# Optimization experiments

Hardware: AMD Instinct MI355X
Metric: run time of the kernel (lower is better)

The kernel has to match this reference:

```python
import jax, jax.numpy as jnp
import numpy as np

N_NODES = 100000
N_GRAPHS = 64


def gcn_conv(x, src, dst, W, b, num_nodes):
    """PyG GCNConv: add self-loops, symmetric deg normalization, aggregate at dst."""
    h = x @ W  # [N, out]
    ones_e = jnp.ones(src.shape[0], dtype=x.dtype)
    # degree includes self-loop (+1)
    deg = jax.ops.segment_sum(ones_e, dst, num_segments=num_nodes) + 1.0
    dinv = jnp.where(deg > 0, 1.0 / jnp.sqrt(deg), 0.0)  # deg>=1 always here
    norm = dinv[src] * dinv[dst]  # [E]
    msg = h[src] * norm[:, None]  # gather + scale
    agg = jax.ops.segment_sum(msg, dst, num_segments=num_nodes)
    # self-loop contribution: norm_ii = dinv[i]^2
    agg = agg + h * (dinv * dinv)[:, None]
    return agg + b


def global_mean_pool(x, batch, num_graphs):
    sums = jax.ops.segment_sum(x, batch, num_segments=num_graphs)
    counts = jax.ops.segment_sum(jnp.ones(x.shape[0], dtype=x.dtype), batch,
                                 num_segments=num_graphs)
    return sums / jnp.maximum(counts, 1.0)[:, None]


def setup_inputs() -> dict:
    key = jax.random.key(0)
    ks = jax.random.split(key, 8)
    H = 128
    x = jax.random.normal(ks[0], (N_NODES, 4), dtype=jnp.float32)
    edge_index = jax.random.randint(ks[1], (2, 1600000), 0, N_NODES, dtype=jnp.int64 if jax.config.read('jax_enable_x64') else jnp.int32)
    batch = jnp.sort(jax.random.randint(ks[2], (N_NODES,), 0, N_GRAPHS))
    def glorot(k, shape):
        fan_in, fan_out = shape
        lim = np.sqrt(6.0 / (fan_in + fan_out))
        return jax.random.uniform(k, shape, jnp.float32, -lim, lim)
    return {
        'x': x,
        'edge_index': edge_index,
        'batch': batch,
        'W1': glorot(ks[3], (4, H)), 'b1': jnp.zeros((H,), jnp.float32),
        'W2': glorot(ks[4], (H, H)), 'b2': jnp.zeros((H,), jnp.float32),
        'W3': glorot(ks[5], (H, H)), 'b3': jnp.zeros((H,), jnp.float32),
        'Wl': glorot(ks[6], (H, 2)), 'bl': jnp.zeros((2,), jnp.float32),
    }


def reference(x, edge_index, batch, W1, b1, W2, b2, W3, b3, Wl, bl):
    src, dst = edge_index[0], edge_index[1]
    h = jax.nn.relu(gcn_conv(x, src, dst, W1, b1, N_NODES))
    h = jax.nn.relu(gcn_conv(h, src, dst, W2, b2, N_NODES))
    h = jax.nn.relu(gcn_conv(h, src, dst, W3, b3, N_NODES))
    g = global_mean_pool(h, batch, N_GRAPHS)  # [G, H]
    logits = g @ Wl + bl  # [G, 2]
    return jax.nn.log_softmax(logits, axis=1)
```

## Files before the change

kernel.cpp:

```cpp
#include <hip/hip_runtime.h>

#define HDIM 128
#define NGRAPH 64

#define BSHIFT 9
#define NBUCK 196
#define BCAP 84
#define BSTR 85
#define RCAP 9216
#define BIN_CHUNK 8192

typedef __attribute__((ext_vector_type(8))) short short8;
typedef __attribute__((ext_vector_type(4))) float floatx4;
typedef __attribute__((ext_vector_type(2))) float floatx2;
typedef __attribute__((ext_vector_type(4))) unsigned int uintx4;

__device__ __forceinline__ float bf2f(unsigned short u) {
    union { unsigned int i; float f; } v;
    v.i = ((unsigned int)u) << 16;
    return v.f;
}
__device__ __forceinline__ unsigned short f2bf(float f) {
    unsigned int u = __float_as_uint(f);
    u += 0x7FFFu + ((u >> 16) & 1u);
    return (unsigned short)(u >> 16);
}


__global__ __launch_bounds__(256) void k_misc(int* __restrict__ gcur,
                                              const int* __restrict__ batch,
                                              float* __restrict__ gcnt,
                                              float* __restrict__ gsum,
                                              const float* __restrict__ W2,
                                              unsigned short* __restrict__ Wp2,
                                              const float* __restrict__ W3,
                                              unsigned short* __restrict__ Wp3,
                                              int N, int nbuck) {
    int t = threadIdx.x;
    int blk = blockIdx.x;
    if (blk == 0) {
        if (t < nbuck) gcur[t] = t * RCAP;
        for (int i = t; i < NGRAPH * 128; i += 256) gsum[i] = 0.f;
        if (t < NGRAPH) {
            int g = t;
            int lo = 0, hi = N;
            while (lo < hi) { int m = (lo + hi) >> 1; if (batch[m] < g) lo = m + 1; else hi = m; }
            int lb = lo;
            lo = 0; hi = N;
            while (lo < hi) { int m = (lo + hi) >> 1; if (batch[m] < g + 1) lo = m + 1; else hi = m; }
            gcnt[g] = (float)(lo - lb);
        }
        return;
    }
    const float* W = (blk <= 64) ? W2 : W3;
    unsigned short* Wp = (blk <= 64) ? Wp2 : Wp3;
    int idx = ((blk <= 64) ? (blk - 1) : (blk - 65)) * 256 + t;
    int j = idx & 7, l = (idx >> 3) & 63, frag = idx >> 9;
    int c = frag >> 2, ks = frag & 3;
    int k = ks * 32 + ((l >> 4) & 3) * 8 + j;
    int n = c * 16 + (l & 15);
    Wp[idx] = f2bf(W[k * 128 + n]);
}


__global__ __launch_bounds__(256) void k_binA(const int* __restrict__ src,
                                              const int* __restrict__ dst,
                                              int* __restrict__ gcur,
                                              unsigned int* __restrict__ binned, int E) {
    __shared__ unsigned int bin[NBUCK * BSTR];
    __shared__ int bcnt[NBUCK];
    __shared__ int bbase[NBUCK];
    int t = threadIdx.x;
    for (int b = t; b < NBUCK; b += 256) bcnt[b] = 0;
    __syncthreads();
    int e0 = blockIdx.x * BIN_CHUNK;
    #pragma unroll
    for (int i = 0; i < BIN_CHUNK / 1024; i++) {
        int e = e0 + i * 1024 + t * 4;
        if (e + 3 < E) {
            const int4 d4 = *(const int4*)&dst[e];
            const int4 s4 = *(const int4*)&src[e];
            int dd[4] = {d4.x, d4.y, d4.z, d4.w};
            int ss[4] = {s4.x, s4.y, s4.z, s4.w};
            #pragma unroll
            for (int k = 0; k < 4; k++) {
                int d = dd[k];
                unsigned int rec = ((unsigned int)(d & 511) << 20) | (unsigned int)ss[k];
                int b = d >> BSHIFT;
                int idx = atomicAdd(&bcnt[b], 1);
                if (idx < BCAP) bin[b * BSTR + idx] = rec;
                else { int p = atomicAdd(&gcur[b], 1); binned[p] = rec; }
            }
        } else {
            for (int k = 0; k < 4; k++) {
                int e2 = e + k;
                if (e2 < E) {
                    int d = dst[e2];
                    unsigned int rec = ((unsigned int)(d & 511) << 20) | (unsigned int)src[e2];
                    int b = d >> BSHIFT;
                    int idx = atomicAdd(&bcnt[b], 1);
                    if (idx < BCAP) bin[b * BSTR + idx] = rec;
                    else { int p = atomicAdd(&gcur[b], 1); binned[p] = rec; }
                }
            }
        }
    }
    __syncthreads();
    if (t < NBUCK) {
        int cnt = min(bcnt[t], BCAP);
        bbase[t] = atomicAdd(&gcur[t], cnt);
    }
    __syncthreads();
    int wave = t >> 6, lane = t & 63;
    for (int b = wave; b < NBUCK; b += 4) {
        int cnt = min(bcnt[b], BCAP);
        int base = bbase[b];
        for (int j = lane; j < cnt; j += 64) binned[base + j] = bin[b * BSTR + j];
    }
}

__global__ __launch_bounds__(256) void k_fillB(const int* __restrict__ gcur,
                                               const unsigned int* __restrict__ binned,
                                               int* __restrict__ P,
                                               float* __restrict__ dinv,
                                               int* __restrict__ csr,
                                               const float4* __restrict__ x4,
                                               float4* __restrict__ xs4,
                                               int N, int nbuck) {
    __shared__ int ps[256];
    __shared__ int cnt[512];
    __shared__ int image[RCAP];
    int b = blockIdx.x;
    int t = threadIdx.x;
    int lt = (t < nbuck) ? (gcur[t] - t * RCAP) : 0;
    ps[t] = lt;
    __syncthreads();
    for (int d = 1; d < 256; d <<= 1) {
        int o = (t >= d) ? ps[t - d] : 0;
        __syncthreads();
        ps[t] += o;
        __syncthreads();
    }
    int start = (b > 0) ? ps[b - 1] : 0;
    int len = ps[b] - start;
    __syncthreads();

    int n0 = b << BSHIFT;
    int nloc = min(n0 + 512, N) - n0;
    cnt[t] = 0; cnt[t + 256] = 0;
    __syncthreads();
    const unsigned int* rb = binned + (size_t)b * RCAP;
    for (int i = t; i < len; i += 256) atomicAdd(&cnt[rb[i] >> 20], 1);
    __syncthreads();
    int c0 = cnt[2 * t], c1 = cnt[2 * t + 1];
    int pair = c0 + c1;
    __syncthreads();
    cnt[t] = pair;
    __syncthreads();
    for (int d = 1; d < 256; d <<= 1) {
        int o = (t >= d) ? cnt[t - d] : 0;
        __syncthreads();
        cnt[t] += o;
        __syncthreads();
    }
    int excl = cnt[t] - pair;
    __syncthreads();
    if (2 * t < nloc) {
        int n = n0 + 2 * t;
        float dv0 = rsqrtf((float)c0 + 1.0f);
        P[n] = start + excl;
        dinv[n] = dv0;
        float4 xv = x4[n];
        xs4[n] = make_float4(xv.x * dv0, xv.y * dv0, xv.z * dv0, xv.w * dv0);
    }
    if (2 * t + 1 < nloc) {
        int n = n0 + 2 * t + 1;
        float dv1 = rsqrtf((float)c1 + 1.0f);
        P[n] = start + excl + c0;
        dinv[n] = dv1;
        float4 xv = x4[n];
        xs4[n] = make_float4(xv.x * dv1, xv.y * dv1, xv.z * dv1, xv.w * dv1);
    }
    if (b == nbuck - 1 && t == 0) P[N] = start + len;
    cnt[2 * t] = excl;
    cnt[2 * t + 1] = excl + c0;
    __syncthreads();
    for (int i = t; i < len; i += 256) {
        unsigned int rec = rb[i];
        int pos = atomicAdd(&cnt[rec >> 20], 1);
        image[pos] = (int)(rec & 0xFFFFFu);
    }
    __syncthreads();
    for (int i = t; i < len; i += 256) csr[start + i] = image[i];
}

#define LXS 136
#define LFPS 144
__global__ __launch_bounds__(256) void k_l1t2(const int* __restrict__ P,
                                              const int* __restrict__ csr,
                                              const float4* __restrict__ xs,
                                              const float* __restrict__ W1,
                                              const float* __restrict__ b1,
                                              const unsigned short* __restrict__ Wp,
                                              const float* __restrict__ dinv,
                                              unsigned char* __restrict__ out8, int N) {
    __shared__ unsigned short lx[64 * LXS];
    __shared__ unsigned short lw[16384];
    __shared__ float w1s[512];
    __shared__ float b1s[128];
    __shared__ float ax[64][4];
    int t = threadIdx.x;
    int n0 = blockIdx.x * 64;

    for (int i = t; i < 512; i += 256) w1s[i] = W1[i];
    if (t < 128) b1s[t] = b1[t];
    for (int ch = t; ch < 2048; ch += 256)
        *(uint4*)&lw[ch * 8] = *(const uint4*)&Wp[ch * 8];

    {
        int d = n0 + (t >> 2), l = t & 3;
        float axx = 0.f, ayy = 0.f, azz = 0.f, aww = 0.f;
        if (d < N) {
            int s0 = P[d], s1 = P[d + 1];
            int i = s0 + l;
            for (; i + 4 < s1; i += 8) {
                int e0 = csr[i], e1 = csr[i + 4];
                float4 v0 = xs[e0], v1 = xs[e1];
                axx += v0.x + v1.x; ayy += v0.y + v1.y;
                azz += v0.z + v1.z; aww += v0.w + v1.w;
            }
            if (i < s1) {
                float4 v = xs[csr[i]];
                axx += v.x; ayy += v.y; azz += v.z; aww += v.w;
            }
        }
        axx += __shfl_xor(axx, 1); ayy += __shfl_xor(ayy, 1);
        azz += __shfl_xor(azz, 1); aww += __shfl_xor(aww, 1);
        axx += __shfl_xor(axx, 2); ayy += __shfl_xor(ayy, 2);
        azz += __shfl_xor(azz, 2); aww += __shfl_xor(aww, 2);
        if (l == 0) {
            int nl = t >> 2;
            if (d < N) {
                float dd = dinv[d];
                float4 sv = xs[d];
                ax[nl][0] = (axx + sv.x * dd) * dd;
                ax[nl][1] = (ayy + sv.y * dd) * dd;
                ax[nl][2] = (azz + sv.z * dd) * dd;
                ax[nl][3] = (aww + sv.w * dd) * dd;
            } else {
                ax[nl][0] = 0.f; ax[nl][1] = 0.f; ax[nl][2] = 0.f; ax[nl][3] = 0.f;
            }
        }
    }
    __syncthreads();

    for (int i = t; i < 8192; i += 256) {
        int n = i >> 7, j = i & 127;
        float v = b1s[j] + ax[n][0] * w1s[j] + ax[n][1] * w1s[128 + j]
                         + ax[n][2] * w1s[256 + j] + ax[n][3] * w1s[384 + j];
        lx[n * LXS + j] = f2bf(fmaxf(v, 0.f));
    }
    __syncthreads();

    int w = t >> 6, lane = t & 63;
    int m0 = w * 16;
    int col = lane & 15, quad = lane >> 4;

    short8 afrag[4];
    #pragma unroll
    for (int ks = 0; ks < 4; ks++)
        afrag[ks] = *(const short8*)&lx[(m0 + col) * LXS + ks * 32 + quad * 8];

    float dv[4];
    #pragma unroll
    for (int r = 0; r < 4; r++) {
        int gn = n0 + m0 + quad * 4 + r;
        dv[r] = (gn < N) ? dinv[gn] : 0.0f;
    }
    __syncthreads();
    unsigned char* lfp = (unsigned char*)lx;

    #pragma unroll
    for (int c = 0; c < 8; c++) {
        floatx4 acc = {0.f, 0.f, 0.f, 0.f};
        #pragma unroll
        for (int ks = 0; ks < 4; ks++) {
            const short8 bfrag = *(const short8*)&lw[((c * 4 + ks) * 64 + lane) * 8];
            acc = __builtin_amdgcn_mfma_f32_16x16x32_bf16(afrag[ks], bfrag, acc, 0, 0, 0);
        }
        int j = c * 16 + col;
        #pragma unroll
        for (int r = 0; r < 4; r++) {
            int nl = m0 + quad * 4 + r;
            float v = acc[r] * dv[r];
            lfp[nl * LFPS + j] =
                (unsigned char)(__builtin_amdgcn_cvt_pk_fp8_f32(v, v, 0, false) & 0xFF);
        }
    }
    __syncthreads();
    #pragma unroll
    for (int k = 0; k < 2; k++) {
        int ch = t + k * 256;
        int s = ch >> 7;
        int idx2 = ch & 127;
        int nl = idx2 >> 1;
        int k0 = (idx2 & 1) * 16;
        int gn = n0 + nl;
        if (gn < N)
            *(uintx4*)&out8[(size_t)s * N * 32 + (size_t)gn * 32 + k0] =
                *(const uintx4*)&lfp[nl * LFPS + s * 32 + k0];
    }
}

__global__ __launch_bounds__(256) void k_transform_mfma(const unsigned short* __restrict__ in,
                                                        const unsigned short* __restrict__ Wp,
                                                        const float* __restrict__ dinv,
                                                        unsigned char* __restrict__ out8, int N) {
    __shared__ unsigned short lx[64 * LXS];
    __shared__ unsigned short lw[16384];
    int t = threadIdx.x;
    int n0 = blockIdx.x * 64;

    for (int ch = t; ch < 1024; ch += 256) {
        int row = ch >> 4, part = ch & 15;
        uint4 val = make_uint4(0, 0, 0, 0);
        if (n0 + row < N) val = *(const uint4*)&in[(size_t)(n0 + row) * 128 + part * 8];
        *(uint4*)&lx[row * LXS + part * 8] = val;
    }
    for (int ch = t; ch < 2048; ch += 256)
        *(uint4*)&lw[ch * 8] = *(const uint4*)&Wp[ch * 8];
    __syncthreads();

    int w = t >> 6, lane = t & 63;
    int m0 = w * 16;
    int col = lane & 15, quad = lane >> 4;

    short8 afrag[4];
    #pragma unroll
    for (int ks = 0; ks < 4; ks++)
        afrag[ks] = *(const short8*)&lx[(m0 + col) * LXS + ks * 32 + quad * 8];

    float dv[4];
    #pragma unroll
    for (int r = 0; r < 4; r++) {
        int gn = n0 + m0 + quad * 4 + r;
        dv[r] = (gn < N) ? dinv[gn] : 0.0f;
    }
    __syncthreads();
    unsigned char* lfp = (unsigned char*)lx;

    #pragma unroll
    for (int c = 0; c < 8; c++) {
        floatx4 acc = {0.f, 0.f, 0.f, 0.f};
        #pragma unroll
        for (int ks = 0; ks < 4; ks++) {
            const short8 bfrag = *(const short8*)&lw[((c * 4 + ks) * 64 + lane) * 8];
            acc = __builtin_amdgcn_mfma_f32_16x16x32_bf16(afrag[ks], bfrag, acc, 0, 0, 0);
        }
        int j = c * 16 + col;
        #pragma unroll
        for (int r = 0; r < 4; r++) {
            int nl = m0 + quad * 4 + r;
            float v = acc[r] * dv[r];
            lfp[nl * LFPS + j] =
                (unsigned char)(__builtin_amdgcn_cvt_pk_fp8_f32(v, v, 0, false) & 0xFF);
        }
    }
    __syncthreads();
    #pragma unroll
    for (int k = 0; k < 2; k++) {
        int ch = t + k * 256;
        int s = ch >> 7;
        int idx2 = ch & 127;
        int nl = idx2 >> 1;
        int k0 = (idx2 & 1) * 16;
        int gn = n0 + nl;
        if (gn < N)
            *(uintx4*)&out8[(size_t)s * N * 32 + (size_t)gn * 32 + k0] =
                *(const uintx4*)&lfp[nl * LFPS + s * 32 + k0];
    }
}

__device__ __forceinline__ void dec8x2(uint4 u, floatx2* a) {
    a[0] += __builtin_amdgcn_cvt_pk_f32_fp8(u.x, false);
    a[1] += __builtin_amdgcn_cvt_pk_f32_fp8(u.x, true);
    a[2] += __builtin_amdgcn_cvt_pk_f32_fp8(u.y, false);
    a[3] += __builtin_amdgcn_cvt_pk_f32_fp8(u.y, true);
    a[4] += __builtin_amdgcn_cvt_pk_f32_fp8(u.z, false);
    a[5] += __builtin_amdgcn_cvt_pk_f32_fp8(u.z, true);
    a[6] += __builtin_amdgcn_cvt_pk_f32_fp8(u.w, false);
    a[7] += __builtin_amdgcn_cvt_pk_f32_fp8(u.w, true);
}

__global__ __launch_bounds__(256) void k_agg_sl(const int* __restrict__ P,
                                                const int* __restrict__ csr,
                                                const unsigned int* __restrict__ tab,
                                                const float* __restrict__ dinv,
                                                const float* __restrict__ bias,
                                                unsigned short* __restrict__ out16,
                                                const int* __restrict__ batch,
                                                float* __restrict__ gsum,
                                                int N, int mode) {
    __shared__ float psum[32][32];
    int t = threadIdx.x;
    int bid = blockIdx.x;
    int xcd = bid & 7;
    int slice = xcd >> 1;
    int chunk = (bid >> 3) * 2 + (xcd & 1);
    int nb = chunk * 32;
    int grp = t >> 3;
    int lg = t & 7;
    int slot = lg >> 1;
    int half = lg & 1;
    int g = nb + grp;
    const unsigned int* sl = tab + (size_t)slice * N * 8;
    int hofs = half * 4;

    floatx2 a2[8];
    #pragma unroll
    for (int j = 0; j < 8; j++) a2[j] = (floatx2){0.f, 0.f};

    if (g < N) {
        int s0 = P[g], s1 = P[g + 1];
        int i = s0;
        for (; i + 8 <= s1; i += 8) {
            int e0 = csr[i + slot];
            int e1 = csr[i + slot + 4];
            uint4 u0 = *(const uint4*)&sl[(size_t)e0 * 8 + hofs];
            uint4 u1 = *(const uint4*)&sl[(size_t)e1 * 8 + hofs];
            dec8x2(u0, a2);
            dec8x2(u1, a2);
        }
        if (i + 4 <= s1) {
            int e = csr[i + slot];
            uint4 u = *(const uint4*)&sl[(size_t)e * 8 + hofs];
            dec8x2(u, a2);
            i += 4;
        }
        int k = i + slot;
        if (k < s1) {
            int e = csr[k];
            uint4 u = *(const uint4*)&sl[(size_t)e * 8 + hofs];
            dec8x2(u, a2);
        }
        if (slot == 0) {
            uint4 su = *(const uint4*)&sl[(size_t)g * 8 + hofs];
            dec8x2(su, a2);
        }
    }

    #pragma unroll
    for (int j = 0; j < 8; j++) {
        union { double d; floatx2 f; } u, v;
        u.f = a2[j];
        v.d = __shfl_xor(u.d, 2);
        a2[j] += v.f;
        u.f = a2[j];
        v.d = __shfl_xor(u.d, 4);
        a2[j] += v.f;
    }

    float o[16];
    #pragma unroll
    for (int j = 0; j < 16; j++) o[j] = 0.f;
    if (g < N) {
        float dd = dinv[g];
        const float* bb = &bias[slice * 32 + half * 16];
        #pragma unroll
        for (int j = 0; j < 16; j++) {
            float av = a2[j >> 1][j & 1];
            o[j] = fmaxf(av * dd + bb[j], 0.f);
        }
        if (mode == 0 && slot == 0) {
            uintx4 w0, w1;
            w0.x = (unsigned int)f2bf(o[0]) | ((unsigned int)f2bf(o[1]) << 16);
            w0.y = (unsigned int)f2bf(o[2]) | ((unsigned int)f2bf(o[3]) << 16);
            w0.z = (unsigned int)f2bf(o[4]) | ((unsigned int)f2bf(o[5]) << 16);
            w0.w = (unsigned int)f2bf(o[6]) | ((unsigned int)f2bf(o[7]) << 16);
            w1.x = (unsigned int)f2bf(o[8]) | ((unsigned int)f2bf(o[9]) << 16);
            w1.y = (unsigned int)f2bf(o[10]) | ((unsigned int)f2bf(o[11]) << 16);
            w1.z = (unsigned int)f2bf(o[12]) | ((unsigned int)f2bf(o[13]) << 16);
            w1.w = (unsigned int)f2bf(o[14]) | ((unsigned int)f2bf(o[15]) << 16);
            unsigned short* dst = &out16[(size_t)g * 128 + slice * 32 + half * 16];
            __builtin_nontemporal_store(w0, (uintx4*)dst);
            __builtin_nontemporal_store(w1, (uintx4*)(dst + 8));
        }
    }
    if (mode != 0) {
        if (slot == 0) {
            #pragma unroll
            for (int q = 0; q < 4; q++)
                *(float4*)&psum[grp][half * 16 + q * 4] =
                    make_float4(o[q * 4], o[q * 4 + 1], o[q * 4 + 2], o[q * 4 + 3]);
        }
        __syncthreads();
        if (t < 32 && nb < N) {
            int f = t;
            int nbN = min(32, N - nb);
            int b0 = batch[nb], bL = batch[nb + nbN - 1];
            if (b0 == bL) {
                float s = 0.f;
                #pragma unroll
                for (int n = 0; n < 32; n++) s += psum[n][f];
                unsafeAtomicAdd(&gsum[(size_t)b0 * 128 + slice * 32 + f], s);
            } else {
                float acc = 0.f; int cur = b0;
                for (int n = 0; n < nbN; n++) {
                    int bb = batch[nb + n];
                    if (bb != cur) {
                        unsafeAtomicAdd(&gsum[(size_t)cur * 128 + slice * 32 + f], acc);
                        acc = 0.f; cur = bb;
                    }
                    acc += psum[n][f];
                }
                unsafeAtomicAdd(&gsum[(size_t)cur * 128 + slice * 32 + f], acc);
            }
        }
    }
}

__global__ __launch_bounds__(256) void k_head(const float* __restrict__ gsum,
                                              const float* __restrict__ gcnt,
                                              const float* __restrict__ Wl,
                                              const float* __restrict__ bl,
                                              float* __restrict__ out, int G) {
    int t = threadIdx.x;
    int g = t >> 2, q = t & 3;
    if (g >= G) return;
    float l0 = 0.f, l1 = 0.f;
    #pragma unroll
    for (int k = 0; k < 32; k++) {
        int jj = q * 32 + k;
        float v = gsum[(size_t)g * 128 + jj];
        l0 += v * Wl[jj * 2 + 0];
        l1 += v * Wl[jj * 2 + 1];
    }
    l0 += __shfl_xor(l0, 1, 64); l1 += __shfl_xor(l1, 1, 64);
    l0 += __shfl_xor(l0, 2, 64); l1 += __shfl_xor(l1, 2, 64);
    if (q == 0) {
        float inv = 1.0f / fmaxf(gcnt[g], 1.0f);
        l0 = l0 * inv + bl[0];
        l1 = l1 * inv + bl[1];
        float m = fmaxf(l0, l1);
        float lse = m + logf(expf(l0 - m) + expf(l1 - m));
        out[g * 2 + 0] = l0 - lse;
        out[g * 2 + 1] = l1 - lse;
    }
}


extern "C" void kernel_launch(void* const* d_in, const int* in_sizes, int n_in,
                              void* d_out, int out_size, void* d_ws, size_t ws_size,
                              hipStream_t stream) {
    const float* x   = (const float*)d_in[0];
    const int*   ei  = (const int*)d_in[1];
    const int*   bat = (const int*)d_in[2];
    const float* W1  = (const float*)d_in[3];
    const float* b1  = (const float*)d_in[4];
    const float* W2  = (const float*)d_in[5];
    const float* b2  = (const float*)d_in[6];
    const float* W3  = (const float*)d_in[7];
    const float* b3  = (const float*)d_in[8];
    const float* Wl  = (const float*)d_in[9];
    const float* bl  = (const float*)d_in[10];

    const int N = in_sizes[0] / 4;
    const int E = in_sizes[1] / 2;
    const int* srcI = ei;
    const int* dstI = ei + E;

    const int nbuck = (N + 511) >> BSHIFT;
    const int pAlloc = ((N + 1 + 3) & ~3) + 4;

    float* wsf  = (float*)d_ws;
    float* dinv = wsf;
    int*   P    = (int*)(dinv + N);
    int*   csr  = P + pAlloc;
    float* aggx = (float*)(csr + E);
    unsigned short* bufA16 = (unsigned short*)(aggx + (size_t)N * 4);
    unsigned char*  hs8    = (unsigned char*)(bufA16 + (size_t)N * 128);
    unsigned short* Wp2    = (unsigned short*)(hs8 + (size_t)N * 128);
    unsigned short* Wp3    = Wp2 + 16384;
    float* gsum = (float*)(Wp3 + 16384);
    float* gcnt = gsum + NGRAPH * 128;
    int*   gcur = (int*)(gcnt + NGRAPH);
    unsigned int* binned = (unsigned int*)hs8;
    float* xs4 = (float*)bufA16;

    const int chunks = (N + 31) >> 5;
    const int aggGrid = ((chunks + 1) >> 1) * 8;

    k_misc<<<129, 256, 0, stream>>>(gcur, bat, gcnt, gsum, W2, Wp2, W3, Wp3, N, nbuck);
    k_binA<<<(E + BIN_CHUNK - 1) / BIN_CHUNK, 256, 0, stream>>>(srcI, dstI, gcur, binned, E);
    k_fillB<<<nbuck, 256, 0, stream>>>(gcur, binned, P, dinv, csr,
                                       (const float4*)x, (float4*)xs4, N, nbuck);

    k_l1t2<<<(N + 63) / 64, 256, 0, stream>>>(P, csr, (const float4*)xs4, W1, b1,
                                              Wp2, dinv, hs8, N);

    k_agg_sl<<<aggGrid, 256, 0, stream>>>(P, csr, (const unsigned int*)hs8,
                                          dinv, b2, bufA16, nullptr, nullptr, N, 0);

    k_transform_mfma<<<(N + 63) / 64, 256, 0, stream>>>(bufA16, Wp3, dinv, hs8, N);
    k_agg_sl<<<aggGrid, 256, 0, stream>>>(P, csr, (const unsigned int*)hs8,
                                          dinv, b3, nullptr, bat, gsum, N, 1);

    k_head<<<1, 256, 0, stream>>>(gsum, gcnt, Wl, bl, (float*)d_out, NGRAPH);
}
```

Before: 275.3 us.

## Replace bucketed LDS binning CSR build with global-atomic degree count and scatter

Builds the CSR by counting in-degrees with global atomics, prefix-summing per 512-node block in k_fillP, and scattering src indices with per-node atomic cursors. This replaces the two-pass bucketed binning through shared memory and the per-bucket local sort. It cuts LDS pressure and kernel complexity, but issues 3.2M scattered global atomics. Neighbour order within each row is no longer deterministic, which may hurt the locality of later gathers.

```diff
diff --git a/kernel.cpp b/kernel.cpp
--- a/kernel.cpp
+++ b/kernel.cpp
@@ -2,13 +2,8 @@
 
 #define HDIM 128
 #define NGRAPH 64
-
 #define BSHIFT 9
 #define NBUCK 196
-#define BCAP 84
-#define BSTR 85
-#define RCAP 9216
-#define BIN_CHUNK 8192
 
 typedef __attribute__((ext_vector_type(8))) short short8;
 typedef __attribute__((ext_vector_type(4))) float floatx4;
@@ -27,7 +22,7 @@
 }
 
 
-__global__ __launch_bounds__(256) void k_misc(int* __restrict__ gcur,
+__global__ __launch_bounds__(256) void k_misc(int* __restrict__ deg,
                                               const int* __restrict__ batch,
                                               float* __restrict__ gcnt,
                                               float* __restrict__ gsum,
@@ -35,11 +30,10 @@
                                               unsigned short* __restrict__ Wp2,
                                               const float* __restrict__ W3,
                                               unsigned short* __restrict__ Wp3,
-                                              int N, int nbuck) {
+                                              int N) {
     int t = threadIdx.x;
     int blk = blockIdx.x;
     if (blk == 0) {
-        if (t < nbuck) gcur[t] = t * RCAP;
         for (int i = t; i < NGRAPH * 128; i += 256) gsum[i] = 0.f;
         if (t < NGRAPH) {
             int g = t;
@@ -52,6 +46,12 @@
         }
         return;
     }
+    if (blk >= 129) {
+        int n = ((blk - 129) * 256 + t) * 4;
+        if (n + 3 < N) *(int4*)&deg[n] = make_int4(0, 0, 0, 0);
+        else { for (int k = 0; k < 4; k++) if (n + k < N) deg[n + k] = 0; }
+        return;
+    }
     const float* W = (blk <= 64) ? W2 : W3;
     unsigned short* Wp = (blk <= 64) ? Wp2 : Wp3;
     int idx = ((blk <= 64) ? (blk - 1) : (blk - 65)) * 256 + t;
@@ -63,98 +63,43 @@
 }
 
 
-__global__ __launch_bounds__(256) void k_binA(const int* __restrict__ src,
-                                              const int* __restrict__ dst,
-                                              int* __restrict__ gcur,
-                                              unsigned int* __restrict__ binned, int E) {
-    __shared__ unsigned int bin[NBUCK * BSTR];
-    __shared__ int bcnt[NBUCK];
-    __shared__ int bbase[NBUCK];
-    int t = threadIdx.x;
-    for (int b = t; b < NBUCK; b += 256) bcnt[b] = 0;
-    __syncthreads();
-    int e0 = blockIdx.x * BIN_CHUNK;
-    #pragma unroll
-    for (int i = 0; i < BIN_CHUNK / 1024; i++) {
-        int e = e0 + i * 1024 + t * 4;
-        if (e + 3 < E) {
-            const int4 d4 = *(const int4*)&dst[e];
-            const int4 s4 = *(const int4*)&src[e];
-            int dd[4] = {d4.x, d4.y, d4.z, d4.w};
-            int ss[4] = {s4.x, s4.y, s4.z, s4.w};
-            #pragma unroll
-            for (int k = 0; k < 4; k++) {
-                int d = dd[k];
-                unsigned int rec = ((unsigned int)(d & 511) << 20) | (unsigned int)ss[k];
-                int b = d >> BSHIFT;
-                int idx = atomicAdd(&bcnt[b], 1);
-                if (idx < BCAP) bin[b * BSTR + idx] = rec;
-                else { int p = atomicAdd(&gcur[b], 1); binned[p] = rec; }
-            }
-        } else {
-            for (int k = 0; k < 4; k++) {
-                int e2 = e + k;
-                if (e2 < E) {
-                    int d = dst[e2];
-                    unsigned int rec = ((unsigned int)(d & 511) << 20) | (unsigned int)src[e2];
-                    int b = d >> BSHIFT;
-                    int idx = atomicAdd(&bcnt[b], 1);
-                    if (idx < BCAP) bin[b * BSTR + idx] = rec;
-                    else { int p = atomicAdd(&gcur[b], 1); binned[p] = rec; }
-                }
-            }
-        }
-    }
-    __syncthreads();
-    if (t < NBUCK) {
-        int cnt = min(bcnt[t], BCAP);
-        bbase[t] = atomicAdd(&gcur[t], cnt);
-    }
-    __syncthreads();
-    int wave = t >> 6, lane = t & 63;
-    for (int b = wave; b < NBUCK; b += 4) {
-        int cnt = min(bcnt[b], BCAP);
-        int base = bbase[b];
-        for (int j = lane; j < cnt; j += 64) binned[base + j] = bin[b * BSTR + j];
-    }
-}
-
-__global__ __launch_bounds__(256) void k_fillB(const int* __restrict__ gcur,
-                                               const unsigned int* __restrict__ binned,
+__global__ __launch_bounds__(256) void k_deg(const int* __restrict__ dst,
+                                             int* __restrict__ deg, int E) {
+    int e = (blockIdx.x * 256 + threadIdx.x) * 4;
+    if (e + 3 < E) {
+        const int4 d4 = *(const int4*)&dst[e];
+        atomicAdd(&deg[d4.x], 1); atomicAdd(&deg[d4.y], 1);
+        atomicAdd(&deg[d4.z], 1); atomicAdd(&deg[d4.w], 1);
+    } else {
+        for (int k = 0; k < 4; k++)
+            if (e + k < E) atomicAdd(&deg[dst[e + k]], 1);
+    }
+}
+
+__global__ __launch_bounds__(256) void k_fillP(const int* __restrict__ deg,
                                                int* __restrict__ P,
+                                               int* __restrict__ cur,
                                                float* __restrict__ dinv,
-                                               int* __restrict__ csr,
                                                const float4* __restrict__ x4,
                                                float4* __restrict__ xs4,
                                                int N, int nbuck) {
-    __shared__ int ps[256];
-    __shared__ int cnt[512];
-    __shared__ int image[RCAP];
-    int b = blockIdx.x;
-    int t = threadIdx.x;
-    int lt = (t < nbuck) ? (gcur[t] - t * RCAP) : 0;
-    ps[t] = lt;
-    __syncthreads();
-    for (int d = 1; d < 256; d <<= 1) {
-        int o = (t >= d) ? ps[t - d] : 0;
+    __shared__ int red[256];
+    __shared__ int cnt[256];
+    int b = blockIdx.x, t = threadIdx.x;
+    int n0 = b << BSHIFT;
+    int s = 0;
+    for (int i = t; i < n0; i += 256) s += deg[i];
+    red[t] = s;
+    __syncthreads();
+    for (int d = 128; d > 0; d >>= 1) {
+        if (t < d) red[t] += red[t + d];
         __syncthreads();
-        ps[t] += o;
-        __syncthreads();
-    }
-    int start = (b > 0) ? ps[b - 1] : 0;
-    int len = ps[b] - start;
-    __syncthreads();
-
-    int n0 = b << BSHIFT;
+    }
+    int start = red[0];
     int nloc = min(n0 + 512, N) - n0;
-    cnt[t] = 0; cnt[t + 256] = 0;
-    __syncthreads();
-    const unsigned int* rb = binned + (size_t)b * RCAP;
-    for (int i = t; i < len; i += 256) atomicAdd(&cnt[rb[i] >> 20], 1);
-    __syncthreads();
-    int c0 = cnt[2 * t], c1 = cnt[2 * t + 1];
+    int c0 = (2 * t < nloc) ? deg[n0 + 2 * t] : 0;
+    int c1 = (2 * t + 1 < nloc) ? deg[n0 + 2 * t + 1] : 0;
     int pair = c0 + c1;
-    __syncthreads();
     cnt[t] = pair;
     __syncthreads();
     for (int d = 1; d < 256; d <<= 1) {
@@ -164,34 +109,43 @@
         __syncthreads();
     }
     int excl = cnt[t] - pair;
-    __syncthreads();
     if (2 * t < nloc) {
         int n = n0 + 2 * t;
-        float dv0 = rsqrtf((float)c0 + 1.0f);
-        P[n] = start + excl;
-        dinv[n] = dv0;
+        int p = start + excl;
+        P[n] = p; cur[n] = p;
+        float dv = rsqrtf((float)c0 + 1.0f);
+        dinv[n] = dv;
         float4 xv = x4[n];
-        xs4[n] = make_float4(xv.x * dv0, xv.y * dv0, xv.z * dv0, xv.w * dv0);
+        xs4[n] = make_float4(xv.x * dv, xv.y * dv, xv.z * dv, xv.w * dv);
     }
     if (2 * t + 1 < nloc) {
         int n = n0 + 2 * t + 1;
-        float dv1 = rsqrtf((float)c1 + 1.0f);
-        P[n] = start + excl + c0;
-        dinv[n] = dv1;
+        int p = start + excl + c0;
+        P[n] = p; cur[n] = p;
+        float dv = rsqrtf((float)c1 + 1.0f);
+        dinv[n] = dv;
         float4 xv = x4[n];
-        xs4[n] = make_float4(xv.x * dv1, xv.y * dv1, xv.z * dv1, xv.w * dv1);
-    }
-    if (b == nbuck - 1 && t == 0) P[N] = start + len;
-    cnt[2 * t] = excl;
-    cnt[2 * t + 1] = excl + c0;
-    __syncthreads();
-    for (int i = t; i < len; i += 256) {
-        unsigned int rec = rb[i];
-        int pos = atomicAdd(&cnt[rec >> 20], 1);
-        image[pos] = (int)(rec & 0xFFFFFu);
-    }
-    __syncthreads();
-    for (int i = t; i < len; i += 256) csr[start + i] = image[i];
+        xs4[n] = make_float4(xv.x * dv, xv.y * dv, xv.z * dv, xv.w * dv);
+    }
+    if (b == nbuck - 1 && t == 255) P[N] = start + cnt[255];
+}
+
+__global__ __launch_bounds__(256) void k_scatter(const int* __restrict__ src,
+                                                 const int* __restrict__ dst,
+                                                 int* __restrict__ cur,
+                                                 int* __restrict__ csr, int E) {
+    int e = (blockIdx.x * 256 + threadIdx.x) * 4;
+    if (e + 3 < E) {
+        const int4 d4 = *(const int4*)&dst[e];
+        const int4 s4 = *(const int4*)&src[e];
+        csr[atomicAdd(&cur[d4.x], 1)] = s4.x;
+        csr[atomicAdd(&cur[d4.y], 1)] = s4.y;
+        csr[atomicAdd(&cur[d4.z], 1)] = s4.z;
+        csr[atomicAdd(&cur[d4.w], 1)] = s4.w;
+    } else {
+        for (int k = 0; k < 4; k++)
+            if (e + k < E) csr[atomicAdd(&cur[dst[e + k]], 1)] = src[e + k];
+    }
 }
 
 #define LXS 136
@@ -583,17 +537,21 @@
     unsigned short* Wp3    = Wp2 + 16384;
     float* gsum = (float*)(Wp3 + 16384);
     float* gcnt = gsum + NGRAPH * 128;
-    int*   gcur = (int*)(gcnt + NGRAPH);
-    unsigned int* binned = (unsigned int*)hs8;
-    float* xs4 = (float*)bufA16;
+    int*   deg  = (int*)aggx;
+    int*   cur  = deg + N;
+    float* xs4  = (float*)bufA16;
 
     const int chunks = (N + 31) >> 5;
     const int aggGrid = ((chunks + 1) >> 1) * 8;
-
-    k_misc<<<129, 256, 0, stream>>>(gcur, bat, gcnt, gsum, W2, Wp2, W3, Wp3, N, nbuck);
-    k_binA<<<(E + BIN_CHUNK - 1) / BIN_CHUNK, 256, 0, stream>>>(srcI, dstI, gcur, binned, E);
-    k_fillB<<<nbuck, 256, 0, stream>>>(gcur, binned, P, dinv, csr,
-                                       (const float4*)x, (float4*)xs4, N, nbuck);
+    const int edgeGrid = (E + 1023) / 1024;
+    const int zeroBlocks = (N + 1023) / 1024;
+
+    k_misc<<<129 + zeroBlocks, 256, 0, stream>>>(deg, bat, gcnt, gsum,
+                                                 W2, Wp2, W3, Wp3, N);
+    k_deg<<<edgeGrid, 256, 0, stream>>>(dstI, deg, E);
+    k_fillP<<<nbuck, 256, 0, stream>>>(deg, P, cur, dinv, (const float4*)x,
+                                       (float4*)xs4, N, nbuck);
+    k_scatter<<<edgeGrid, 256, 0, stream>>>(srcI, dstI, cur, csr, E);
 
     k_l1t2<<<(N + 63) / 64, 256, 0, stream>>>(P, csr, (const float4*)xs4, W1, b1,
                                               Wp2, dinv, hs8, N);
```

Measured after the change: 485.0 us. 76.1% more time.
